# Optimization experiments

Measured on AMD Instinct MI355X. Metric: run time of the kernel, lower is better.

Reference implementation:

```python
import jax, jax.numpy as jnp
import numpy as np

B, N, M, F, D = 4, 8, 64, 128, 128
EPS = 1e-5


def setup_inputs() -> dict:
    key = jax.random.key(0)
    ks = jax.random.split(key, 6)
    s1 = 1.0 / np.sqrt(5 * F)
    s2 = 1.0 / np.sqrt(F)
    return {
        "x": jax.random.normal(ks[0], (B, N, M, F), dtype=jnp.float32),
        "W1": jax.random.uniform(ks[1], (F, 5 * F), jnp.float32, -s1, s1),
        "b1": jax.random.uniform(ks[2], (F,), jnp.float32, -s1, s1),
        "gamma": jnp.ones((F,), jnp.float32),
        "beta": jnp.zeros((F,), jnp.float32),
        "bias_p": jax.random.normal(ks[3], (F,), jnp.float32) * 0.02,
        "W2": jax.random.uniform(ks[4], (D, F), jnp.float32, -s2, s2),
        "b2": jax.random.uniform(ks[5], (D,), jnp.float32, -s2, s2),
    }


def reference(x, W1, b1, gamma, beta, bias_p, W2, b2):
    b, n, m, f = x.shape
    e = jnp.eye(m, dtype=x.dtype)[:, :, None]        # (M,M,1) diagonal mask
    xi = x[:, :, :, None, :]                          # value indexed by row i
    xj = x[:, :, None, :, :]                          # value indexed by col j
    mean = jnp.mean(x, axis=2, keepdims=True)[:, :, :, None, :]  # (B,N,1,1,F)
    shp = (b, n, m, m, f)
    # Equivariant 1->2 lift: [diag(x), row-bcast, col-bcast, diag(mean), mean-bcast]
    xAll = jnp.concatenate([
        xi * e,
        jnp.broadcast_to(xi, shp),
        jnp.broadcast_to(xj, shp),
        jnp.broadcast_to(mean * e, shp),
        jnp.broadcast_to(mean, shp),
    ], axis=-1)                                       # (B,N,M,M,5F)
    h = jnp.einsum('bnijk,fk->bnijf', xAll, W1) + b1  # fc1
    mu = jnp.mean(h, axis=-1, keepdims=True)
    var = jnp.mean((h - mu) ** 2, axis=-1, keepdims=True)
    h = (h - mu) / jnp.sqrt(var + EPS) * gamma + beta # LayerNorm
    h = jax.nn.relu(h)
    h = h + bias_p * e                                # diagonal-masked bias
    return jnp.einsum('bnijf,df->bnijd', h, W2) + b2  # fc2 -> (B,N,M,M,D)
```

## Files before the change

kernel.cpp:

```cpp
#include <hip/hip_runtime.h>

typedef __bf16 bf16x4 __attribute__((ext_vector_type(4)));
typedef __bf16 bf16x8 __attribute__((ext_vector_type(8)));
typedef float  f32x4v __attribute__((ext_vector_type(4)));

#define HS 136


__global__ __launch_bounds__(256) void k1_prep(
    const float* __restrict__ x, const float* __restrict__ W1,
    const float* __restrict__ b1, const float* __restrict__ W2,
    float* __restrict__ Up, float* __restrict__ V, float* __restrict__ Dg,
    __bf16* __restrict__ W2b)
{
  __shared__ __align__(16) __bf16 Xhi[64 * HS];
  __shared__ __align__(16) __bf16 Xlo[64 * HS];
  __shared__ float msum[128], pm[256], mw[128];

  const int tid  = threadIdx.x;
  const int bn   = blockIdx.x / 6;
  const int ch   = blockIdx.x % 6;
  const int lane = tid & 63;
  const int w    = tid >> 6;
  const int pidx = ch >> 1;

  if (tid < 128) msum[tid] = 0.f;
  __syncthreads();

  {
    const float4* xv = reinterpret_cast<const float4*>(x + (size_t)bn * 8192);
    const int c = tid & 31;
    float4 ps = {0.f, 0.f, 0.f, 0.f};
#pragma unroll
    for (int it = 0; it < 8; ++it) {
      int p = tid + 256 * it;
      int r = p >> 5;
      float4 v = xv[p];
      ps.x += v.x; ps.y += v.y; ps.z += v.z; ps.w += v.w;
      bf16x4 hv, lv;
      hv[0] = (__bf16)v.x; lv[0] = (__bf16)(v.x - (float)hv[0]);
      hv[1] = (__bf16)v.y; lv[1] = (__bf16)(v.y - (float)hv[1]);
      hv[2] = (__bf16)v.z; lv[2] = (__bf16)(v.z - (float)hv[2]);
      hv[3] = (__bf16)v.w; lv[3] = (__bf16)(v.w - (float)hv[3]);
      *reinterpret_cast<bf16x4*>(&Xhi[r * HS + 4 * c]) = hv;
      *reinterpret_cast<bf16x4*>(&Xlo[r * HS + 4 * c]) = lv;
    }
    atomicAdd(&msum[4 * c + 0], ps.x);
    atomicAdd(&msum[4 * c + 1], ps.y);
    atomicAdd(&msum[4 * c + 2], ps.z);
    atomicAdd(&msum[4 * c + 3], ps.w);
  }

  if (ch == 4) {
    const float4* w2v = reinterpret_cast<const float4*>(W2);
#pragma unroll
    for (int it = 0; it < 16; ++it) {
      int p = tid + 256 * it;
      float4 v = w2v[p];
      bf16x4 hv;
      hv[0] = (__bf16)v.x; hv[1] = (__bf16)v.y;
      hv[2] = (__bf16)v.z; hv[3] = (__bf16)v.w;
      reinterpret_cast<bf16x4*>(W2b)[p] = hv;
    }
  }
  __syncthreads();

  {
    const int f  = tid & 127;
    const int hh = tid >> 7;
    float acc = 0.f;
    if (pidx < 2) {
      const float4* wv4 = reinterpret_cast<const float4*>(
          W1 + (size_t)f * 640 + (pidx == 0 ? 384 : 512) + hh * 64);
#pragma unroll
      for (int kc = 0; kc < 16; ++kc) {
        float4 wv = wv4[kc];
        int k = hh * 64 + 4 * kc;
        acc += msum[k] * wv.x + msum[k + 1] * wv.y +
               msum[k + 2] * wv.z + msum[k + 3] * wv.w;
      }
    }
    pm[tid] = acc;
  }
  __syncthreads();
  if (tid < 128)
    mw[tid] = (pm[tid] + pm[tid + 128]) * (1.f / 64.f) +
              (pidx == 1 ? b1[tid] : 0.f);
  __syncthreads();

  const int m    = lane & 15;
  const int quad = lane >> 4;
  bf16x8 ahi[4], alo[4];
#pragma unroll
  for (int ks = 0; ks < 4; ++ks) {
    ahi[ks] = *reinterpret_cast<const bf16x8*>(&Xhi[(16 * w + m) * HS + 32 * ks + 8 * quad]);
    alo[ks] = *reinterpret_cast<const bf16x8*>(&Xlo[(16 * w + m) * HS + 32 * ks + 8 * quad]);
  }

  float* rout = (pidx == 0) ? Dg : (pidx == 1 ? Up : V);
#pragma unroll
  for (int tt = 0; tt < 4; ++tt) {
    const int fout = (((4 * ch + tt) & 7) * 16) + m;
    const float* wrow = W1 + (size_t)fout * 640 + pidx * 128;
    f32x4v a = {0.f, 0.f, 0.f, 0.f};
#pragma unroll
    for (int ks = 0; ks < 4; ++ks) {
      float4 w0 = *reinterpret_cast<const float4*>(wrow + 32 * ks + 8 * quad);
      float4 w1 = *reinterpret_cast<const float4*>(wrow + 32 * ks + 8 * quad + 4);
      bf16x8 bhi, blo;
      bhi[0] = (__bf16)w0.x; blo[0] = (__bf16)(w0.x - (float)bhi[0]);
      bhi[1] = (__bf16)w0.y; blo[1] = (__bf16)(w0.y - (float)bhi[1]);
      bhi[2] = (__bf16)w0.z; blo[2] = (__bf16)(w0.z - (float)bhi[2]);
      bhi[3] = (__bf16)w0.w; blo[3] = (__bf16)(w0.w - (float)bhi[3]);
      bhi[4] = (__bf16)w1.x; blo[4] = (__bf16)(w1.x - (float)bhi[4]);
      bhi[5] = (__bf16)w1.y; blo[5] = (__bf16)(w1.y - (float)bhi[5]);
      bhi[6] = (__bf16)w1.z; blo[6] = (__bf16)(w1.z - (float)bhi[6]);
      bhi[7] = (__bf16)w1.w; blo[7] = (__bf16)(w1.w - (float)bhi[7]);
      a = __builtin_amdgcn_mfma_f32_16x16x32_bf16(ahi[ks], bhi, a, 0, 0, 0);
      a = __builtin_amdgcn_mfma_f32_16x16x32_bf16(alo[ks], bhi, a, 0, 0, 0);
      a = __builtin_amdgcn_mfma_f32_16x16x32_bf16(ahi[ks], blo, a, 0, 0, 0);
    }
    const float addv = mw[fout];
#pragma unroll
    for (int rg = 0; rg < 4; ++rg) {
      int ii = 16 * w + 4 * quad + rg;
      rout[((size_t)bn * 64 + ii) * 128 + fout] = a[rg] + addv;
    }
  }
}

__global__ __launch_bounds__(256) void k2_main(
    const float* __restrict__ Up, const float* __restrict__ V,
    const float* __restrict__ Dg, const __bf16* __restrict__ W2b,
    const float* __restrict__ gamma, const float* __restrict__ beta,
    const float* __restrict__ bias_p, const float* __restrict__ b2,
    float* __restrict__ out)
{
  __shared__ __align__(16) __bf16 W2s[128 * HS];
  __shared__ __align__(16) __bf16 Hs[64 * HS];

  const int tid  = threadIdx.x;
  const int bid  = blockIdx.x;
  const int bn   = bid >> 6;
  const int i    = bid & 63;
  const int lane = tid & 63;
  const int w    = tid >> 6;

  {
    const uint4* w2v = reinterpret_cast<const uint4*>(W2b);
#pragma unroll
    for (int it = 0; it < 8; ++it) {
      int p   = tid + 256 * it;
      int row = p >> 4;
      int col = (p & 15) * 8;
      *reinterpret_cast<uint4*>(&W2s[row * HS + col]) = w2v[p];
    }
  }

  {
    const int c    = lane & 31;
    const int half = lane >> 5;
    const size_t base = (size_t)bn * 64;
    const float4 up4 = reinterpret_cast<const float4*>(Up + (base + i) * 128)[c];
    const float4 dg4 = reinterpret_cast<const float4*>(Dg + (base + i) * 128)[c];
    const float4 g4  = reinterpret_cast<const float4*>(gamma)[c];
    const float4 be4 = reinterpret_cast<const float4*>(beta)[c];
    const float4 bp4 = reinterpret_cast<const float4*>(bias_p)[c];
    float4 v4s[8];
#pragma unroll
    for (int it = 0; it < 8; ++it) {
      int r = 8 * it + 2 * w + half;
      v4s[it] = reinterpret_cast<const float4*>(V + (base + r) * 128)[c];
    }
#pragma unroll
    for (int it = 0; it < 8; ++it) {
      int r = 8 * it + 2 * w + half;
      float4 v4 = v4s[it];
      float h0 = v4.x + up4.x, h1 = v4.y + up4.y;
      float h2 = v4.z + up4.z, h3 = v4.w + up4.w;
      if (r == i) { h0 += dg4.x; h1 += dg4.y; h2 += dg4.z; h3 += dg4.w; }
      float s = h0 + h1 + h2 + h3;
      float q = h0 * h0 + h1 * h1 + h2 * h2 + h3 * h3;
#pragma unroll
      for (int off = 16; off > 0; off >>= 1) {
        s += __shfl_xor(s, off, 32);
        q += __shfl_xor(q, off, 32);
      }
      float mu   = s * (1.f / 128.f);
      float var  = q * (1.f / 128.f) - mu * mu;
      float rstd = rsqrtf(var + 1e-5f);
      h0 = fmaxf(fmaf((h0 - mu) * rstd, g4.x, be4.x), 0.f);
      h1 = fmaxf(fmaf((h1 - mu) * rstd, g4.y, be4.y), 0.f);
      h2 = fmaxf(fmaf((h2 - mu) * rstd, g4.z, be4.z), 0.f);
      h3 = fmaxf(fmaf((h3 - mu) * rstd, g4.w, be4.w), 0.f);
      if (r == i) { h0 += bp4.x; h1 += bp4.y; h2 += bp4.z; h3 += bp4.w; }
      bf16x4 hv;
      hv[0] = (__bf16)h0; hv[1] = (__bf16)h1;
      hv[2] = (__bf16)h2; hv[3] = (__bf16)h3;
      *reinterpret_cast<bf16x4*>(&Hs[r * HS + 4 * c]) = hv;
    }
  }
  __syncthreads();

  const int m    = lane & 15;
  const int quad = lane >> 4;
  bf16x8 af[4];
#pragma unroll
  for (int ks = 0; ks < 4; ++ks)
    af[ks] = *reinterpret_cast<const bf16x8*>(
        &Hs[(16 * w + m) * HS + 32 * ks + 8 * quad]);

  const size_t obase = (size_t)bid * 8192;
#pragma unroll
  for (int t = 0; t < 8; ++t) {
    f32x4v a = {0.f, 0.f, 0.f, 0.f};
#pragma unroll
    for (int ks = 0; ks < 4; ++ks) {
      bf16x8 bf = *reinterpret_cast<const bf16x8*>(
          &W2s[(16 * t + m) * HS + 32 * ks + 8 * quad]);
      a = __builtin_amdgcn_mfma_f32_16x16x32_bf16(af[ks], bf, a, 0, 0, 0);
    }
    const int d = 16 * t + m;
    const float b2v = b2[d];
#pragma unroll
    for (int rg = 0; rg < 4; ++rg) {
      int j = 16 * w + 4 * quad + rg;
      out[obase + (size_t)j * 128 + d] = a[rg] + b2v;
    }
  }
}

extern "C" void kernel_launch(void* const* d_in, const int* in_sizes, int n_in,
                              void* d_out, int out_size, void* d_ws, size_t ws_size,
                              hipStream_t stream) {
  const float* x      = (const float*)d_in[0];
  const float* W1     = (const float*)d_in[1];
  const float* b1     = (const float*)d_in[2];
  const float* gamma  = (const float*)d_in[3];
  const float* beta   = (const float*)d_in[4];
  const float* bias_p = (const float*)d_in[5];
  const float* W2     = (const float*)d_in[6];
  const float* b2     = (const float*)d_in[7];

  float*  Up  = (float*)d_ws;
  float*  V   = Up + 2048 * 128;
  float*  Dg  = V + 2048 * 128;
  __bf16* W2b = (__bf16*)(Dg + 2048 * 128);

  k1_prep<<<192, 256, 0, stream>>>(x, W1, b1, W2, Up, V, Dg, W2b);
  k2_main<<<2048, 256, 0, stream>>>(Up, V, Dg, W2b, gamma, beta, bias_p, b2,
                                    (float*)d_out);
}
```

Measured before the change: 110.7 us.

## Read W2 fragments from global memory and swap MFMA operands for vector stores

The main kernel no longer stages the bf16 W2 matrix into shared memory. Each MFMA reads its W2 fragment straight from global memory, which should stay cache-resident. The MFMA operands are swapped so each lane holds four consecutive output columns, so the results and b2 can be stored and loaded as float4. This removes a 34KB shared-memory fill and its LDS footprint, which may raise occupancy, and turns scalar strided output stores into vectorized ones. The cost is repeated global or L2 loads of W2 inside the inner loop.

```diff
diff --git a/kernel.cpp b/kernel.cpp
--- a/kernel.cpp
+++ b/kernel.cpp
@@ -136,7 +136,6 @@
     const float* __restrict__ bias_p, const float* __restrict__ b2,
     float* __restrict__ out)
 {
-  __shared__ __align__(16) __bf16 W2s[128 * HS];
   __shared__ __align__(16) __bf16 Hs[64 * HS];
 
   const int tid  = threadIdx.x;
@@ -145,17 +144,6 @@
   const int i    = bid & 63;
   const int lane = tid & 63;
   const int w    = tid >> 6;
-
-  {
-    const uint4* w2v = reinterpret_cast<const uint4*>(W2b);
-#pragma unroll
-    for (int it = 0; it < 8; ++it) {
-      int p   = tid + 256 * it;
-      int row = p >> 4;
-      int col = (p & 15) * 8;
-      *reinterpret_cast<uint4*>(&W2s[row * HS + col]) = w2v[p];
-    }
-  }
 
   {
     const int c    = lane & 31;
@@ -204,29 +192,29 @@
 
   const int m    = lane & 15;
   const int quad = lane >> 4;
-  bf16x8 af[4];
+  bf16x8 bh[4];
 #pragma unroll
   for (int ks = 0; ks < 4; ++ks)
-    af[ks] = *reinterpret_cast<const bf16x8*>(
+    bh[ks] = *reinterpret_cast<const bf16x8*>(
         &Hs[(16 * w + m) * HS + 32 * ks + 8 * quad]);
 
   const size_t obase = (size_t)bid * 8192;
+  const float* orow  = out + obase + (size_t)(16 * w + m) * 128;
 #pragma unroll
   for (int t = 0; t < 8; ++t) {
     f32x4v a = {0.f, 0.f, 0.f, 0.f};
 #pragma unroll
     for (int ks = 0; ks < 4; ++ks) {
-      bf16x8 bf = *reinterpret_cast<const bf16x8*>(
-          &W2s[(16 * t + m) * HS + 32 * ks + 8 * quad]);
-      a = __builtin_amdgcn_mfma_f32_16x16x32_bf16(af[ks], bf, a, 0, 0, 0);
-    }
-    const int d = 16 * t + m;
-    const float b2v = b2[d];
-#pragma unroll
-    for (int rg = 0; rg < 4; ++rg) {
-      int j = 16 * w + 4 * quad + rg;
-      out[obase + (size_t)j * 128 + d] = a[rg] + b2v;
-    }
+      bf16x8 aw = *reinterpret_cast<const bf16x8*>(
+          &W2b[(size_t)(16 * t + m) * 128 + 32 * ks + 8 * quad]);
+      a = __builtin_amdgcn_mfma_f32_16x16x32_bf16(aw, bh[ks], a, 0, 0, 0);
+    }
+    const float4 b2v = *reinterpret_cast<const float4*>(b2 + 16 * t + 4 * quad);
+    float4 o;
+    o.x = a[0] + b2v.x; o.y = a[1] + b2v.y;
+    o.z = a[2] + b2v.z; o.w = a[3] + b2v.w;
+    *reinterpret_cast<float4*>(
+        const_cast<float*>(orow) + 16 * t + 4 * quad) = o;
   }
 }
 
```

New measurement: 132.9 us. 20.0% more time.
